# Optimization experiments

Hardware: AMD Instinct MI355X
Metric: run time of the kernel (lower is better)

The kernel has to match this reference:

```python
import jax, jax.numpy as jnp
import numpy as np

# Dimensions: batch B, window W (time features), nodes M, hidden HID, hops NLAYERS
B, W, M, HID, NLAYERS = 32, 168, 2048, 128, 6


def setup_inputs() -> dict:
    key = jax.random.key(0)
    ks = jax.random.split(key, 6)
    x = jax.random.normal(ks[0], (B, W, M), dtype=jnp.float32)
    # scale L so matrix powers L^k stay bounded (spectral radius < 1)
    L = jax.random.normal(ks[1], (M, M), dtype=jnp.float32) / (2.0 * np.float32(np.sqrt(M)))
    # stacked per-hop MLP params: linears[i]: W->HID, linears2[i]: HID->1
    W1 = jax.random.normal(ks[2], (NLAYERS + 1, HID, W), dtype=jnp.float32) / np.float32(np.sqrt(W))
    b1 = jax.random.normal(ks[3], (NLAYERS + 1, HID), dtype=jnp.float32) * 0.01
    W2 = jax.random.normal(ks[4], (NLAYERS + 1, HID), dtype=jnp.float32) / np.float32(np.sqrt(HID))
    b2 = jax.random.normal(ks[5], (NLAYERS + 1,), dtype=jnp.float32) * 0.01
    return {"x": x, "L": L, "W1": W1, "b1": b1, "W2": W2, "b2": b2}


def _hop_mlp(t, w1, bb1, w2, bb2):
    # t: [B, M, W] -> scalar score per node: Linear(W->HID), ReLU, Linear(HID->1)
    h = jax.nn.relu(jnp.einsum('bmw,hw->bmh', t, w1) + bb1)
    return jnp.einsum('bmh,h->bm', h, w2) + bb2


def reference(x, L, W1, b1, W2, b2):
    xt = jnp.swapaxes(x, 1, 2)  # [B, M, W] (x.transpose(2,1))
    s = _hop_mlp(xt, W1[0], b1[0], W2[0], b2[0])  # [B, M]
    P = L
    for i in range(1, NLAYERS + 1):
        # PP.expand + bmm == broadcasted matmul; never materialize [B,M,M]
        t = jnp.einsum('ij,bjw->biw', P, xt)  # [B, M, W]
        s = s + _hop_mlp(t, W1[i], b1[i], W2[i], b2[i])
        P = jnp.matmul(L, P)  # next graph power
    return s  # [B, M]; output_fun is None so no final nonlinearity
```

## Files before the change

kernel.cpp:

```cpp
#include <hip/hip_runtime.h>
#include <cstdint>
#include <cstddef>

typedef __bf16 bf16_t;
typedef __attribute__((ext_vector_type(8))) __bf16 bf16x8;
typedef __attribute__((ext_vector_type(4))) __bf16 bf16x4;
typedef __attribute__((ext_vector_type(4))) float floatx4;

#define NB 32
#define NW 168
#define NM 2048
#define NHID 128
#define NBW (NB * NW)

#define GLOAD_LDS16(g, l)                                          \
  __builtin_amdgcn_global_load_lds(                                \
      (const __attribute__((address_space(1))) void*)(g),          \
      (__attribute__((address_space(3))) void*)(l), 16, 0, 0)

__global__ void cast_bf16_kernel(const float* __restrict__ in, bf16_t* __restrict__ out, int n4) {
  int stride = gridDim.x * blockDim.x;
  for (int i = blockIdx.x * blockDim.x + threadIdx.x; i < n4; i += stride) {
    float4 v = ((const float4*)in)[i];
    bf16x4 o = {(bf16_t)v.x, (bf16_t)v.y, (bf16_t)v.z, (bf16_t)v.w};
    ((bf16x4*)out)[i] = o;
  }
}

__global__ void prep_x_kernel(const float* __restrict__ x, bf16_t* __restrict__ Xb,
                              bf16_t* __restrict__ XT) {
  __shared__ float tile[64][65];
  const int R = NBW, C = NM;
  int r0 = blockIdx.y * 64, c0 = blockIdx.x * 64;
  int t = threadIdx.x;
  int tr = t >> 4, tc4 = (t & 15) * 4;
#pragma unroll
  for (int p = 0; p < 4; ++p) {
    int row = p * 16 + tr;
    float4 v = *(const float4*)(x + (size_t)(r0 + row) * C + c0 + tc4);
    tile[row][tc4 + 0] = v.x;
    tile[row][tc4 + 1] = v.y;
    tile[row][tc4 + 2] = v.z;
    tile[row][tc4 + 3] = v.w;
    bf16x4 o = {(bf16_t)v.x, (bf16_t)v.y, (bf16_t)v.z, (bf16_t)v.w};
    *(bf16x4*)(Xb + (size_t)(r0 + row) * C + c0 + tc4) = o;
  }
  __syncthreads();
#pragma unroll
  for (int p = 0; p < 4; ++p) {
    int c = p * 16 + tr;
    bf16x4 o = {(bf16_t)tile[tc4 + 0][c], (bf16_t)tile[tc4 + 1][c],
                (bf16_t)tile[tc4 + 2][c], (bf16_t)tile[tc4 + 3][c]};
    *(bf16x4*)(XT + (size_t)(c0 + c) * R + r0 + tc4) = o;
  }
}

__global__ void gemm_nt_kernel(const bf16_t* __restrict__ A, const bf16_t* __restrict__ Bt,
                               bf16_t* __restrict__ C, bf16_t* __restrict__ Ct,
                               int K, int lda, int ldb, int ldc, int ldct, int write_c) {
  __shared__ bf16_t As[128 * 32];
  __shared__ bf16_t Bs[128 * 32];
  int tid = threadIdx.x;
  int m0 = blockIdx.y * 128, n0 = blockIdx.x * 128;
  int lane = tid & 63, wv = tid >> 6;
  int wm = wv >> 1, wn = wv & 1;
  int quad = lane >> 4, l15 = lane & 15;

  int p0 = wv * 128 + lane;
  int p1 = p0 + 64;
  int row0 = p0 >> 2, kc0 = (p0 & 3) ^ ((p0 >> 3) & 3);
  int row1 = p1 >> 2, kc1 = (p1 & 3) ^ ((p1 >> 3) & 3);
  const bf16_t* a0p = A + (size_t)(m0 + row0) * lda + kc0 * 8;
  const bf16_t* a1p = A + (size_t)(m0 + row1) * lda + kc1 * 8;
  const bf16_t* b0p = Bt + (size_t)(n0 + row0) * ldb + kc0 * 8;
  const bf16_t* b1p = Bt + (size_t)(n0 + row1) * ldb + kc1 * 8;
  bf16_t* As_d0 = As + (size_t)(wv * 128) * 8;
  bf16_t* As_d1 = As + (size_t)(wv * 128 + 64) * 8;
  bf16_t* Bs_d0 = Bs + (size_t)(wv * 128) * 8;
  bf16_t* Bs_d1 = Bs + (size_t)(wv * 128 + 64) * 8;

  int swz = (l15 >> 1) & 3;
  int kpos = (quad ^ swz) * 8;

  floatx4 zero4 = {0.f, 0.f, 0.f, 0.f};
  floatx4 acc[4][4];
#pragma unroll
  for (int mi = 0; mi < 4; ++mi)
#pragma unroll
    for (int ni = 0; ni < 4; ++ni) acc[mi][ni] = zero4;

  for (int kb = 0; kb < K; kb += 32) {
    GLOAD_LDS16(a0p + kb, As_d0);
    GLOAD_LDS16(a1p + kb, As_d1);
    GLOAD_LDS16(b0p + kb, Bs_d0);
    GLOAD_LDS16(b1p + kb, Bs_d1);
    __syncthreads();
    bf16x8 af[4], bf[4];
#pragma unroll
    for (int mi = 0; mi < 4; ++mi)
      af[mi] = *(const bf16x8*)(As + (wm * 64 + mi * 16 + l15) * 32 + kpos);
#pragma unroll
    for (int ni = 0; ni < 4; ++ni)
      bf[ni] = *(const bf16x8*)(Bs + (wn * 64 + ni * 16 + l15) * 32 + kpos);
#pragma unroll
    for (int mi = 0; mi < 4; ++mi)
#pragma unroll
      for (int ni = 0; ni < 4; ++ni)
        acc[mi][ni] = __builtin_amdgcn_mfma_f32_16x16x32_bf16(af[mi], bf[ni], acc[mi][ni], 0, 0, 0);
    __syncthreads();
  }
#pragma unroll
  for (int mi = 0; mi < 4; ++mi) {
#pragma unroll
    for (int ni = 0; ni < 4; ++ni) {
      int col = n0 + wn * 64 + ni * 16 + l15;
      int rowb = m0 + wm * 64 + mi * 16 + quad * 4;
      bf16x4 tv;
#pragma unroll
      for (int r = 0; r < 4; ++r) tv[r] = (bf16_t)acc[mi][ni][r];
      *(bf16x4*)(Ct + (size_t)col * ldct + rowb) = tv;
      if (write_c) {
#pragma unroll
        for (int r = 0; r < 4; ++r)
          C[(size_t)(rowb + r) * ldc + col] = tv[r];
      }
    }
  }
}

__global__ void mlp_score_kernel(const bf16_t* __restrict__ T, const bf16_t* __restrict__ W1b,
                                 const float* __restrict__ b1, const float* __restrict__ W2,
                                 const float* __restrict__ b2, float* __restrict__ out,
                                 int hop, int accumulate) {
  __shared__ bf16_t Bs[24 * 128 * 8];
  __shared__ float sred[4][64];
  const bf16_t* Wh = W1b + (size_t)hop * NHID * NW;
  const float* b1h = b1 + hop * NHID;
  const float* w2h = W2 + hop * NHID;
  int tid = threadIdx.x;
  int r0 = blockIdx.x * 128;
  int lane = tid & 63, wv = tid >> 6;
  int wm = wv >> 1, wn = wv & 1;
  int quad = lane >> 4, l15 = lane & 15;

  for (int c = 2688 + tid; c < 3072; c += 256) {
    int4 z = {0, 0, 0, 0};
    *(int4*)(Bs + (size_t)c * 8) = z;
  }
  for (int i = 0; i < 11; ++i) {
    int c = i * 256 + tid;
    if (c < 2688) {
      int kc = c >> 7;
      int h = (c & 127) ^ ((kc & 3) << 2);
      GLOAD_LDS16(Wh + (size_t)h * NW + kc * 8, Bs + (size_t)(i * 256 + wv * 64) * 8);
    }
  }

  const bf16_t* arow[4];
#pragma unroll
  for (int mi = 0; mi < 4; ++mi) {
    int R = r0 + wm * 64 + mi * 16 + l15;
    arow[mi] = T + (size_t)(R >> 5) * NBW + (size_t)(R & 31) * NW + quad * 8;
  }

  floatx4 zero4 = {0.f, 0.f, 0.f, 0.f};
  floatx4 acc[4][4];
#pragma unroll
  for (int mi = 0; mi < 4; ++mi)
#pragma unroll
    for (int ni = 0; ni < 4; ++ni) acc[mi][ni] = zero4;

  __syncthreads();

#pragma unroll
  for (int kb = 0; kb < 192; kb += 32) {
    int kc = (kb >> 3) + quad;
    bf16x8 af[4], bf[4];
#pragma unroll
    for (int mi = 0; mi < 4; ++mi)
      af[mi] = *(const bf16x8*)(arow[mi] + kb);
#pragma unroll
    for (int ni = 0; ni < 4; ++ni) {
      int hpos = (wn * 64 + ni * 16 + l15) ^ ((kc & 3) << 2);
      bf[ni] = *(const bf16x8*)(Bs + (size_t)(kc * 128 + hpos) * 8);
    }
#pragma unroll
    for (int mi = 0; mi < 4; ++mi)
#pragma unroll
      for (int ni = 0; ni < 4; ++ni)
        acc[mi][ni] = __builtin_amdgcn_mfma_f32_16x16x32_bf16(af[mi], bf[ni], acc[mi][ni], 0, 0, 0);
  }

  float part[4][4];
#pragma unroll
  for (int mi = 0; mi < 4; ++mi)
#pragma unroll
    for (int r = 0; r < 4; ++r) part[mi][r] = 0.f;
#pragma unroll
  for (int ni = 0; ni < 4; ++ni) {
    int col = wn * 64 + ni * 16 + l15;
    float b1v = b1h[col];
    float w2v = w2h[col];
#pragma unroll
    for (int mi = 0; mi < 4; ++mi)
#pragma unroll
      for (int r = 0; r < 4; ++r) {
        float h = acc[mi][ni][r] + b1v;
        h = h > 0.f ? h : 0.f;
        part[mi][r] += h * w2v;
      }
  }
#pragma unroll
  for (int off = 1; off < 16; off <<= 1)
#pragma unroll
    for (int mi = 0; mi < 4; ++mi)
#pragma unroll
      for (int r = 0; r < 4; ++r) part[mi][r] += __shfl_xor(part[mi][r], off);
  if (l15 == 0) {
#pragma unroll
    for (int mi = 0; mi < 4; ++mi)
#pragma unroll
      for (int r = 0; r < 4; ++r) sred[wv][mi * 16 + quad * 4 + r] = part[mi][r];
  }
  __syncthreads();
  if (tid < 128) {
    int half = tid >> 6;
    int lr = tid & 63;
    float v = sred[half * 2][lr] + sred[half * 2 + 1][lr] + b2[hop];
    int R = r0 + half * 64 + lr;
    int idx = (R & 31) * NM + (R >> 5);
    if (accumulate)
      out[idx] += v;
    else
      out[idx] = v;
  }
}

extern "C" void kernel_launch(void* const* d_in, const int* in_sizes, int n_in,
                              void* d_out, int out_size, void* d_ws, size_t ws_size,
                              hipStream_t stream) {
  const float* x = (const float*)d_in[0];
  const float* L = (const float*)d_in[1];
  const float* W1 = (const float*)d_in[2];
  const float* b1 = (const float*)d_in[3];
  const float* W2 = (const float*)d_in[4];
  const float* b2 = (const float*)d_in[5];
  float* out = (float*)d_out;

  char* ws = (char*)d_ws;
  size_t off = 0;
  auto walloc = [&](size_t bytes) -> void* {
    off = (off + 255) & ~(size_t)255;
    void* p = ws + off;
    off += bytes;
    return p;
  };
  bf16_t* Xb = (bf16_t*)walloc((size_t)NBW * NM * 2);
  bf16_t* XT = (bf16_t*)walloc((size_t)NM * NBW * 2);
  bf16_t* Lb = (bf16_t*)walloc((size_t)NM * NM * 2);
  bf16_t* W1b = (bf16_t*)walloc((size_t)7 * NHID * NW * 2);
  bf16_t* Ta = (bf16_t*)walloc((size_t)NBW * NM * 2);
  (void)ws_size; (void)in_sizes; (void)n_in; (void)out_size;

  prep_x_kernel<<<dim3(NM / 64, NBW / 64), dim3(256), 0, stream>>>(x, Xb, XT);
  cast_bf16_kernel<<<dim3(1024), dim3(256), 0, stream>>>(L, Lb, NM * NM / 4);
  cast_bf16_kernel<<<dim3(64), dim3(256), 0, stream>>>(W1, W1b, 7 * NHID * NW / 4);

  mlp_score_kernel<<<dim3(NM * NB / 128), dim3(256), 0, stream>>>(XT, W1b, b1, W2, b2, out, 0, 0);

  bf16_t* src = Xb;
  bf16_t* dst = Ta;
  for (int i = 1; i <= 6; ++i) {
    gemm_nt_kernel<<<dim3(NM / 128, NBW / 128), dim3(256), 0, stream>>>(
        src, Lb, dst, XT, NM, NM, NM, NM, NBW, (i < 6) ? 1 : 0);
    mlp_score_kernel<<<dim3(NM * NB / 128), dim3(256), 0, stream>>>(XT, W1b, b1, W2, b2, out, i, 1);
    bf16_t* t = src; src = dst; dst = t;
  }
}
```

Before: 552.7 us.

## Batch hops by precomputing powers of L and fusing multi-hop GEMMs and MLPs

Replaces the six sequential propagation GEMMs with three wider launches. It computes L^2 and L^3 on spare blocks and multiplies by a stacked [L, L^2, L^3] so several hops come out of one GEMM. The MLP scoring is batched over two or three hops per launch and accumulates with atomicAdd into a zero-initialised output. This cuts serial dependency depth and launch count and gives the GPU larger grids, at the cost of extra GEMM work for the matrix powers. It also adds extra bf16 rounding through the precomputed powers.

```diff
diff --git a/kernel.cpp b/kernel.cpp
--- a/kernel.cpp
+++ b/kernel.cpp
@@ -24,6 +24,31 @@
     float4 v = ((const float4*)in)[i];
     bf16x4 o = {(bf16_t)v.x, (bf16_t)v.y, (bf16_t)v.z, (bf16_t)v.w};
     ((bf16x4*)out)[i] = o;
+  }
+}
+
+__global__ void transpose_cast_kernel(const float* __restrict__ in, bf16_t* __restrict__ out,
+                                      int R, int C) {
+  __shared__ float tile[64][65];
+  int r0 = blockIdx.y * 64, c0 = blockIdx.x * 64;
+  int t = threadIdx.x;
+  int tr = t >> 4, tc4 = (t & 15) * 4;
+#pragma unroll
+  for (int p = 0; p < 4; ++p) {
+    int row = p * 16 + tr;
+    float4 v = *(const float4*)(in + (size_t)(r0 + row) * C + c0 + tc4);
+    tile[row][tc4 + 0] = v.x;
+    tile[row][tc4 + 1] = v.y;
+    tile[row][tc4 + 2] = v.z;
+    tile[row][tc4 + 3] = v.w;
+  }
+  __syncthreads();
+#pragma unroll
+  for (int p = 0; p < 4; ++p) {
+    int c = p * 16 + tr;
+    bf16x4 o = {(bf16_t)tile[tc4 + 0][c], (bf16_t)tile[tc4 + 1][c],
+                (bf16_t)tile[tc4 + 2][c], (bf16_t)tile[tc4 + 3][c]};
+    *(bf16x4*)(out + (size_t)(c0 + c) * R + r0 + tc4) = o;
   }
 }
 
@@ -55,13 +80,35 @@
   }
 }
 
-__global__ void gemm_nt_kernel(const bf16_t* __restrict__ A, const bf16_t* __restrict__ Bt,
-                               bf16_t* __restrict__ C, bf16_t* __restrict__ Ct,
-                               int K, int lda, int ldb, int ldc, int ldct, int write_c) {
+template <int MODE>
+__global__ void gemm_multi(const bf16_t* __restrict__ A, const bf16_t* __restrict__ Bt,
+                           const bf16_t* __restrict__ A2, const bf16_t* __restrict__ Bt2,
+                           bf16_t* __restrict__ C, bf16_t* __restrict__ Caux,
+                           bf16_t* __restrict__ Ct0, bf16_t* __restrict__ Ct1,
+                           bf16_t* __restrict__ Ct2) {
+  constexpr int NBX = (MODE == 0) ? 16 : (MODE == 1) ? 32 : 48;
+  constexpr int NMAIN = 42 * NBX;
   __shared__ bf16_t As[128 * 32];
   __shared__ bf16_t Bs[128 * 32];
+  int bid = blockIdx.x;
   int tid = threadIdx.x;
-  int m0 = blockIdx.y * 128, n0 = blockIdx.x * 128;
+  const bf16_t* Ap;
+  const bf16_t* Btp;
+  int m0, n0;
+  bool aux = false;
+  if (MODE < 2 && bid >= NMAIN) {
+    aux = true;
+    int l = bid - NMAIN;
+    m0 = (l >> 4) * 128;
+    n0 = (l & 15) * 128;
+    Ap = A2;
+    Btp = Bt2;
+  } else {
+    m0 = (bid / NBX) * 128;
+    n0 = (bid % NBX) * 128;
+    Ap = A;
+    Btp = Bt;
+  }
   int lane = tid & 63, wv = tid >> 6;
   int wm = wv >> 1, wn = wv & 1;
   int quad = lane >> 4, l15 = lane & 15;
@@ -70,10 +117,10 @@
   int p1 = p0 + 64;
   int row0 = p0 >> 2, kc0 = (p0 & 3) ^ ((p0 >> 3) & 3);
   int row1 = p1 >> 2, kc1 = (p1 & 3) ^ ((p1 >> 3) & 3);
-  const bf16_t* a0p = A + (size_t)(m0 + row0) * lda + kc0 * 8;
-  const bf16_t* a1p = A + (size_t)(m0 + row1) * lda + kc1 * 8;
-  const bf16_t* b0p = Bt + (size_t)(n0 + row0) * ldb + kc0 * 8;
-  const bf16_t* b1p = Bt + (size_t)(n0 + row1) * ldb + kc1 * 8;
+  const bf16_t* a0p = Ap + (size_t)(m0 + row0) * 2048 + kc0 * 8;
+  const bf16_t* a1p = Ap + (size_t)(m0 + row1) * 2048 + kc1 * 8;
+  const bf16_t* b0p = Btp + (size_t)(n0 + row0) * 2048 + kc0 * 8;
+  const bf16_t* b1p = Btp + (size_t)(n0 + row1) * 2048 + kc1 * 8;
   bf16_t* As_d0 = As + (size_t)(wv * 128) * 8;
   bf16_t* As_d1 = As + (size_t)(wv * 128 + 64) * 8;
   bf16_t* Bs_d0 = Bs + (size_t)(wv * 128) * 8;
@@ -89,7 +136,7 @@
 #pragma unroll
     for (int ni = 0; ni < 4; ++ni) acc[mi][ni] = zero4;
 
-  for (int kb = 0; kb < K; kb += 32) {
+  for (int kb = 0; kb < 2048; kb += 32) {
     GLOAD_LDS16(a0p + kb, As_d0);
     GLOAD_LDS16(a1p + kb, As_d1);
     GLOAD_LDS16(b0p + kb, Bs_d0);
@@ -109,36 +156,50 @@
         acc[mi][ni] = __builtin_amdgcn_mfma_f32_16x16x32_bf16(af[mi], bf[ni], acc[mi][ni], 0, 0, 0);
     __syncthreads();
   }
+
+  int nh = n0 >> 11;
+  int n0l = n0 - (nh << 11);
+  bf16_t* Ctp = nullptr;
+  bf16_t* Cp = nullptr;
+  if (aux) {
+    Cp = Caux;
+  } else {
+    Ctp = (nh == 0) ? Ct0 : (nh == 1) ? Ct1 : Ct2;
+    if (MODE == 0) Cp = C;
+    if (MODE == 1 && nh == 1) Cp = C;
+  }
 #pragma unroll
   for (int mi = 0; mi < 4; ++mi) {
 #pragma unroll
     for (int ni = 0; ni < 4; ++ni) {
-      int col = n0 + wn * 64 + ni * 16 + l15;
+      int col_l = n0l + wn * 64 + ni * 16 + l15;
       int rowb = m0 + wm * 64 + mi * 16 + quad * 4;
       bf16x4 tv;
 #pragma unroll
       for (int r = 0; r < 4; ++r) tv[r] = (bf16_t)acc[mi][ni][r];
-      *(bf16x4*)(Ct + (size_t)col * ldct + rowb) = tv;
-      if (write_c) {
-#pragma unroll
-        for (int r = 0; r < 4; ++r)
-          C[(size_t)(rowb + r) * ldc + col] = tv[r];
+      if (Ctp) *(bf16x4*)(Ctp + (size_t)col_l * NBW + rowb) = tv;
+      if (Cp) {
+#pragma unroll
+        for (int r = 0; r < 4; ++r) Cp[(size_t)(rowb + r) * 2048 + col_l] = tv[r];
       }
     }
   }
 }
 
-__global__ void mlp_score_kernel(const bf16_t* __restrict__ T, const bf16_t* __restrict__ W1b,
-                                 const float* __restrict__ b1, const float* __restrict__ W2,
-                                 const float* __restrict__ b2, float* __restrict__ out,
-                                 int hop, int accumulate) {
+__global__ void mlp_multi(const bf16_t* __restrict__ T0, const bf16_t* __restrict__ T1,
+                          const bf16_t* __restrict__ T2, const bf16_t* __restrict__ W1b,
+                          const float* __restrict__ b1, const float* __restrict__ W2,
+                          const float* __restrict__ b2, float* __restrict__ out, int hop_base) {
   __shared__ bf16_t Bs[24 * 128 * 8];
   __shared__ float sred[4][64];
+  int sub = blockIdx.x >> 9;
+  int r0 = (blockIdx.x & 511) * 128;
+  int hop = hop_base + sub;
+  const bf16_t* T = (sub == 0) ? T0 : (sub == 1) ? T1 : T2;
   const bf16_t* Wh = W1b + (size_t)hop * NHID * NW;
   const float* b1h = b1 + hop * NHID;
   const float* w2h = W2 + hop * NHID;
   int tid = threadIdx.x;
-  int r0 = blockIdx.x * 128;
   int lane = tid & 63, wv = tid >> 6;
   int wm = wv >> 1, wn = wv & 1;
   int quad = lane >> 4, l15 = lane & 15;
@@ -229,10 +290,7 @@
     float v = sred[half * 2][lr] + sred[half * 2 + 1][lr] + b2[hop];
     int R = r0 + half * 64 + lr;
     int idx = (R & 31) * NM + (R >> 5);
-    if (accumulate)
-      out[idx] += v;
-    else
-      out[idx] = v;
+    atomicAdd(out + idx, v);
   }
 }
 
@@ -255,25 +313,35 @@
     off += bytes;
     return p;
   };
-  bf16_t* Xb = (bf16_t*)walloc((size_t)NBW * NM * 2);
-  bf16_t* XT = (bf16_t*)walloc((size_t)NM * NBW * 2);
-  bf16_t* Lb = (bf16_t*)walloc((size_t)NM * NM * 2);
+  const size_t SZ_L = (size_t)NM * NM * 2;
+  const size_t SZ_T = (size_t)NBW * NM * 2;
   bf16_t* W1b = (bf16_t*)walloc((size_t)7 * NHID * NW * 2);
-  bf16_t* Ta = (bf16_t*)walloc((size_t)NBW * NM * 2);
-  (void)ws_size; (void)in_sizes; (void)n_in; (void)out_size;
-
-  prep_x_kernel<<<dim3(NM / 64, NBW / 64), dim3(256), 0, stream>>>(x, Xb, XT);
+  bf16_t* Lstack = (bf16_t*)walloc(3 * SZ_L);
+  bf16_t* Lb = Lstack;
+  bf16_t* L2b = Lstack + (size_t)NM * NM;
+  bf16_t* L3b = Lstack + 2 * (size_t)NM * NM;
+  bf16_t* Ltb = (bf16_t*)walloc(SZ_L);
+  bf16_t* Tt1 = (bf16_t*)walloc(SZ_T);
+  bf16_t* XTp2 = (bf16_t*)((char*)Ltb);
+  bf16_t* Xb = (bf16_t*)walloc(SZ_T);
+  bf16_t* Tt3 = Xb;
+  bf16_t* XTp0 = (bf16_t*)walloc(SZ_T);
+  bf16_t* XTp1 = (bf16_t*)walloc(SZ_T);
+  (void)ws_size; (void)in_sizes; (void)n_in;
+
+  hipMemsetAsync(out, 0, (size_t)out_size * 4, stream);
+  prep_x_kernel<<<dim3(NM / 64, NBW / 64), dim3(256), 0, stream>>>(x, Xb, XTp0);
   cast_bf16_kernel<<<dim3(1024), dim3(256), 0, stream>>>(L, Lb, NM * NM / 4);
+  transpose_cast_kernel<<<dim3(NM / 64, NM / 64), dim3(256), 0, stream>>>(L, Ltb, NM, NM);
   cast_bf16_kernel<<<dim3(64), dim3(256), 0, stream>>>(W1, W1b, 7 * NHID * NW / 4);
 
-  mlp_score_kernel<<<dim3(NM * NB / 128), dim3(256), 0, stream>>>(XT, W1b, b1, W2, b2, out, 0, 0);
-
-  bf16_t* src = Xb;
-  bf16_t* dst = Ta;
-  for (int i = 1; i <= 6; ++i) {
-    gemm_nt_kernel<<<dim3(NM / 128, NBW / 128), dim3(256), 0, stream>>>(
-        src, Lb, dst, XT, NM, NM, NM, NM, NBW, (i < 6) ? 1 : 0);
-    mlp_score_kernel<<<dim3(NM * NB / 128), dim3(256), 0, stream>>>(XT, W1b, b1, W2, b2, out, i, 1);
-    bf16_t* t = src; src = dst; dst = t;
-  }
-}
+  gemm_multi<0><<<dim3(928), dim3(256), 0, stream>>>(
+      Xb, Lb, Lb, Ltb, Tt1, L2b, XTp1, nullptr, nullptr);
+  mlp_multi<<<dim3(1024), dim3(256), 0, stream>>>(XTp0, XTp1, nullptr, W1b, b1, W2, b2, out, 0);
+  gemm_multi<1><<<dim3(1600), dim3(256), 0, stream>>>(
+      Tt1, Lstack, L2b, Ltb, Tt3, L3b, XTp0, XTp1, nullptr);
+  mlp_multi<<<dim3(1024), dim3(256), 0, stream>>>(XTp0, XTp1, nullptr, W1b, b1, W2, b2, out, 2);
+  gemm_multi<2><<<dim3(2016), dim3(256), 0, stream>>>(
+      Tt3, Lstack, nullptr, nullptr, nullptr, nullptr, XTp0, XTp1, XTp2);
+  mlp_multi<<<dim3(1536), dim3(256), 0, stream>>>(XTp0, XTp1, XTp2, W1b, b1, W2, b2, out, 4);
+}
```

Measured after the change: 561.6 us. No clear change (+1.6%).

## Overlap each hop's GEMM with previous hop's MLP scoring in one launch

Applied to the files above, without the earlier changes.

Merges the three prep kernels into one launch and repacks W1 into a zero-padded 192-wide bf16 layout. Each hop now runs one kernel where the first 672 blocks compute the next graph-propagation GEMM while the remaining 512 blocks score the previous hop's output through the MLP. XT buffers are double-buffered so both halves can run at once. This cuts the launch count and fills idle CUs during the GEMM, at the cost of extra workspace and MLP blocks that read W1 straight from global memory instead of staging it in LDS.

```diff
diff --git a/kernel.cpp b/kernel.cpp
--- a/kernel.cpp
+++ b/kernel.cpp
@@ -12,76 +12,85 @@
 #define NM 2048
 #define NHID 128
 #define NBW (NB * NW)
+#define GEMM_BLOCKS 672
 
 #define GLOAD_LDS16(g, l)                                          \
   __builtin_amdgcn_global_load_lds(                                \
       (const __attribute__((address_space(1))) void*)(g),          \
       (__attribute__((address_space(3))) void*)(l), 16, 0, 0)
 
-__global__ void cast_bf16_kernel(const float* __restrict__ in, bf16_t* __restrict__ out, int n4) {
-  int stride = gridDim.x * blockDim.x;
-  for (int i = blockIdx.x * blockDim.x + threadIdx.x; i < n4; i += stride) {
-    float4 v = ((const float4*)in)[i];
-    bf16x4 o = {(bf16_t)v.x, (bf16_t)v.y, (bf16_t)v.z, (bf16_t)v.w};
-    ((bf16x4*)out)[i] = o;
+__global__ void prep_all(const float* __restrict__ x, bf16_t* __restrict__ Xb,
+                         bf16_t* __restrict__ XT, const float* __restrict__ L,
+                         bf16_t* __restrict__ Lb, const float* __restrict__ W1,
+                         bf16_t* __restrict__ W1p) {
+  __shared__ float tile[64][65];
+  int bid = blockIdx.x;
+  int t = threadIdx.x;
+  if (bid < 2688) {
+    const int C = NM;
+    int r0 = (bid >> 5) * 64, c0 = (bid & 31) * 64;
+    int tr = t >> 4, tc4 = (t & 15) * 4;
+#pragma unroll
+    for (int p = 0; p < 4; ++p) {
+      int row = p * 16 + tr;
+      float4 v = *(const float4*)(x + (size_t)(r0 + row) * C + c0 + tc4);
+      tile[row][tc4 + 0] = v.x;
+      tile[row][tc4 + 1] = v.y;
+      tile[row][tc4 + 2] = v.z;
+      tile[row][tc4 + 3] = v.w;
+      bf16x4 o = {(bf16_t)v.x, (bf16_t)v.y, (bf16_t)v.z, (bf16_t)v.w};
+      *(bf16x4*)(Xb + (size_t)(r0 + row) * C + c0 + tc4) = o;
+    }
+    __syncthreads();
+#pragma unroll
+    for (int p = 0; p < 4; ++p) {
+      int c = p * 16 + tr;
+      bf16x4 o = {(bf16_t)tile[tc4 + 0][c], (bf16_t)tile[tc4 + 1][c],
+                  (bf16_t)tile[tc4 + 2][c], (bf16_t)tile[tc4 + 3][c]};
+      *(bf16x4*)(XT + (size_t)(c0 + c) * NBW + r0 + tc4) = o;
+    }
+  } else if (bid < 3200) {
+    int i = (bid - 2688) * 256 + t;
+    const int n4 = NM * NM / 4;
+    const int stride = 512 * 256;
+    for (; i < n4; i += stride) {
+      float4 v = ((const float4*)L)[i];
+      bf16x4 o = {(bf16_t)v.x, (bf16_t)v.y, (bf16_t)v.z, (bf16_t)v.w};
+      ((bf16x4*)Lb)[i] = o;
+    }
+  } else {
+    int hop = bid - 3200;
+    const float* src = W1 + (size_t)hop * NHID * NW;
+    bf16_t* dst = W1p + (size_t)hop * NHID * 192;
+    for (int c = t; c < 3072; c += 256) {
+      int h = c / 24, kc = c % 24;
+      bf16x8 o;
+      if (kc < 21) {
+        const float* s = src + (size_t)h * NW + kc * 8;
+#pragma unroll
+        for (int j = 0; j < 8; ++j) o[j] = (bf16_t)s[j];
+      } else {
+#pragma unroll
+        for (int j = 0; j < 8; ++j) o[j] = (bf16_t)0.0f;
+      }
+      *(bf16x8*)(dst + (size_t)h * 192 + kc * 8) = o;
+    }
   }
 }
 
-__global__ void prep_x_kernel(const float* __restrict__ x, bf16_t* __restrict__ Xb,
-                              bf16_t* __restrict__ XT) {
-  __shared__ float tile[64][65];
-  const int R = NBW, C = NM;
-  int r0 = blockIdx.y * 64, c0 = blockIdx.x * 64;
-  int t = threadIdx.x;
-  int tr = t >> 4, tc4 = (t & 15) * 4;
-#pragma unroll
-  for (int p = 0; p < 4; ++p) {
-    int row = p * 16 + tr;
-    float4 v = *(const float4*)(x + (size_t)(r0 + row) * C + c0 + tc4);
-    tile[row][tc4 + 0] = v.x;
-    tile[row][tc4 + 1] = v.y;
-    tile[row][tc4 + 2] = v.z;
-    tile[row][tc4 + 3] = v.w;
-    bf16x4 o = {(bf16_t)v.x, (bf16_t)v.y, (bf16_t)v.z, (bf16_t)v.w};
-    *(bf16x4*)(Xb + (size_t)(r0 + row) * C + c0 + tc4) = o;
-  }
-  __syncthreads();
-#pragma unroll
-  for (int p = 0; p < 4; ++p) {
-    int c = p * 16 + tr;
-    bf16x4 o = {(bf16_t)tile[tc4 + 0][c], (bf16_t)tile[tc4 + 1][c],
-                (bf16_t)tile[tc4 + 2][c], (bf16_t)tile[tc4 + 3][c]};
-    *(bf16x4*)(XT + (size_t)(c0 + c) * R + r0 + tc4) = o;
-  }
-}
-
-__global__ void gemm_nt_kernel(const bf16_t* __restrict__ A, const bf16_t* __restrict__ Bt,
-                               bf16_t* __restrict__ C, bf16_t* __restrict__ Ct,
-                               int K, int lda, int ldb, int ldc, int ldct, int write_c) {
+__global__ void fused_hop(const bf16_t* __restrict__ A, const bf16_t* __restrict__ Lb,
+                          bf16_t* __restrict__ Tt, bf16_t* __restrict__ XTout,
+                          const bf16_t* __restrict__ XTin, const bf16_t* __restrict__ W1p,
+                          const float* __restrict__ b1, const float* __restrict__ W2,
+                          const float* __restrict__ b2, float* __restrict__ out,
+                          int hop, int accumulate, int gemm_blocks, int write_c) {
   __shared__ bf16_t As[128 * 32];
   __shared__ bf16_t Bs[128 * 32];
+  __shared__ float sred[4][64];
   int tid = threadIdx.x;
-  int m0 = blockIdx.y * 128, n0 = blockIdx.x * 128;
   int lane = tid & 63, wv = tid >> 6;
   int wm = wv >> 1, wn = wv & 1;
   int quad = lane >> 4, l15 = lane & 15;
-
-  int p0 = wv * 128 + lane;
-  int p1 = p0 + 64;
-  int row0 = p0 >> 2, kc0 = (p0 & 3) ^ ((p0 >> 3) & 3);
-  int row1 = p1 >> 2, kc1 = (p1 & 3) ^ ((p1 >> 3) & 3);
-  const bf16_t* a0p = A + (size_t)(m0 + row0) * lda + kc0 * 8;
-  const bf16_t* a1p = A + (size_t)(m0 + row1) * lda + kc1 * 8;
-  const bf16_t* b0p = Bt + (size_t)(n0 + row0) * ldb + kc0 * 8;
-  const bf16_t* b1p = Bt + (size_t)(n0 + row1) * ldb + kc1 * 8;
-  bf16_t* As_d0 = As + (size_t)(wv * 128) * 8;
-  bf16_t* As_d1 = As + (size_t)(wv * 128 + 64) * 8;
-  bf16_t* Bs_d0 = Bs + (size_t)(wv * 128) * 8;
-  bf16_t* Bs_d1 = Bs + (size_t)(wv * 128 + 64) * 8;
-
-  int swz = (l15 >> 1) & 3;
-  int kpos = (quad ^ swz) * 8;
-
   floatx4 zero4 = {0.f, 0.f, 0.f, 0.f};
   floatx4 acc[4][4];
 #pragma unroll
@@ -89,150 +98,135 @@
 #pragma unroll
     for (int ni = 0; ni < 4; ++ni) acc[mi][ni] = zero4;
 
-  for (int kb = 0; kb < K; kb += 32) {
-    GLOAD_LDS16(a0p + kb, As_d0);
-    GLOAD_LDS16(a1p + kb, As_d1);
-    GLOAD_LDS16(b0p + kb, Bs_d0);
-    GLOAD_LDS16(b1p + kb, Bs_d1);
+  if ((int)blockIdx.x < gemm_blocks) {
+    int bid = blockIdx.x;
+    int m0 = (bid >> 4) * 128, n0 = (bid & 15) * 128;
+    int p0 = wv * 128 + lane;
+    int p1 = p0 + 64;
+    int row0 = p0 >> 2, kc0 = (p0 & 3) ^ ((p0 >> 3) & 3);
+    int row1 = p1 >> 2, kc1 = (p1 & 3) ^ ((p1 >> 3) & 3);
+    const bf16_t* a0p = A + (size_t)(m0 + row0) * NM + kc0 * 8;
+    const bf16_t* a1p = A + (size_t)(m0 + row1) * NM + kc1 * 8;
+    const bf16_t* b0p = Lb + (size_t)(n0 + row0) * NM + kc0 * 8;
+    const bf16_t* b1p = Lb + (size_t)(n0 + row1) * NM + kc1 * 8;
+    bf16_t* As_d0 = As + (size_t)(wv * 128) * 8;
+    bf16_t* As_d1 = As + (size_t)(wv * 128 + 64) * 8;
+    bf16_t* Bs_d0 = Bs + (size_t)(wv * 128) * 8;
+    bf16_t* Bs_d1 = Bs + (size_t)(wv * 128 + 64) * 8;
+    int swz = (l15 >> 1) & 3;
+    int kpos = (quad ^ swz) * 8;
+
+    for (int kb = 0; kb < 2048; kb += 32) {
+      GLOAD_LDS16(a0p + kb, As_d0);
+      GLOAD_LDS16(a1p + kb, As_d1);
+      GLOAD_LDS16(b0p + kb, Bs_d0);
+      GLOAD_LDS16(b1p + kb, Bs_d1);
+      __syncthreads();
+      bf16x8 af[4], bf[4];
+#pragma unroll
+      for (int mi = 0; mi < 4; ++mi)
+        af[mi] = *(const bf16x8*)(As + (wm * 64 + mi * 16 + l15) * 32 + kpos);
+#pragma unroll
+      for (int ni = 0; ni < 4; ++ni)
+        bf[ni] = *(const bf16x8*)(Bs + (wn * 64 + ni * 16 + l15) * 32 + kpos);
+#pragma unroll
+      for (int mi = 0; mi < 4; ++mi)
+#pragma unroll
+        for (int ni = 0; ni < 4; ++ni)
+          acc[mi][ni] =
+              __builtin_amdgcn_mfma_f32_16x16x32_bf16(af[mi], bf[ni], acc[mi][ni], 0, 0, 0);
+      __syncthreads();
+    }
+#pragma unroll
+    for (int mi = 0; mi < 4; ++mi) {
+#pragma unroll
+      for (int ni = 0; ni < 4; ++ni) {
+        int col = n0 + wn * 64 + ni * 16 + l15;
+        int rowb = m0 + wm * 64 + mi * 16 + quad * 4;
+        bf16x4 tv;
+#pragma unroll
+        for (int r = 0; r < 4; ++r) tv[r] = (bf16_t)acc[mi][ni][r];
+        *(bf16x4*)(XTout + (size_t)col * NBW + rowb) = tv;
+        if (write_c) {
+#pragma unroll
+          for (int r = 0; r < 4; ++r) Tt[(size_t)(rowb + r) * NM + col] = tv[r];
+        }
+      }
+    }
+  } else {
+    int bid2 = blockIdx.x - gemm_blocks;
+    int r0 = bid2 * 128;
+    const bf16_t* Wh = W1p + (size_t)hop * NHID * 192;
+    const float* b1h = b1 + hop * NHID;
+    const float* w2h = W2 + hop * NHID;
+    const bf16_t* arow[4];
+#pragma unroll
+    for (int mi = 0; mi < 4; ++mi) {
+      int R = r0 + wm * 64 + mi * 16 + l15;
+      arow[mi] = XTin + (size_t)(R >> 5) * NBW + (size_t)(R & 31) * NW + quad * 8;
+    }
+#pragma unroll
+    for (int kb = 0; kb < 192; kb += 32) {
+      int kc = (kb >> 3) + quad;
+      bf16x8 af[4], bf[4];
+#pragma unroll
+      for (int mi = 0; mi < 4; ++mi)
+        af[mi] = *(const bf16x8*)(arow[mi] + kb);
+#pragma unroll
+      for (int ni = 0; ni < 4; ++ni) {
+        int h = wn * 64 + ni * 16 + l15;
+        bf[ni] = *(const bf16x8*)(Wh + (size_t)h * 192 + kc * 8);
+      }
+#pragma unroll
+      for (int mi = 0; mi < 4; ++mi)
+#pragma unroll
+        for (int ni = 0; ni < 4; ++ni)
+          acc[mi][ni] =
+              __builtin_amdgcn_mfma_f32_16x16x32_bf16(af[mi], bf[ni], acc[mi][ni], 0, 0, 0);
+    }
+    float part[4][4];
+#pragma unroll
+    for (int mi = 0; mi < 4; ++mi)
+#pragma unroll
+      for (int r = 0; r < 4; ++r) part[mi][r] = 0.f;
+#pragma unroll
+    for (int ni = 0; ni < 4; ++ni) {
+      int col = wn * 64 + ni * 16 + l15;
+      float b1v = b1h[col];
+      float w2v = w2h[col];
+#pragma unroll
+      for (int mi = 0; mi < 4; ++mi)
+#pragma unroll
+        for (int r = 0; r < 4; ++r) {
+          float h = acc[mi][ni][r] + b1v;
+          h = h > 0.f ? h : 0.f;
+          part[mi][r] += h * w2v;
+        }
+    }
+#pragma unroll
+    for (int off = 1; off < 16; off <<= 1)
+#pragma unroll
+      for (int mi = 0; mi < 4; ++mi)
+#pragma unroll
+        for (int r = 0; r < 4; ++r) part[mi][r] += __shfl_xor(part[mi][r], off);
+    if (l15 == 0) {
+#pragma unroll
+      for (int mi = 0; mi < 4; ++mi)
+#pragma unroll
+        for (int r = 0; r < 4; ++r) sred[wv][mi * 16 + quad * 4 + r] = part[mi][r];
+    }
     __syncthreads();
-    bf16x8 af[4], bf[4];
-#pragma unroll
-    for (int mi = 0; mi < 4; ++mi)
-      af[mi] = *(const bf16x8*)(As + (wm * 64 + mi * 16 + l15) * 32 + kpos);
-#pragma unroll
-    for (int ni = 0; ni < 4; ++ni)
-      bf[ni] = *(const bf16x8*)(Bs + (wn * 64 + ni * 16 + l15) * 32 + kpos);
-#pragma unroll
-    for (int mi = 0; mi < 4; ++mi)
-#pragma unroll
-      for (int ni = 0; ni < 4; ++ni)
-        acc[mi][ni] = __builtin_amdgcn_mfma_f32_16x16x32_bf16(af[mi], bf[ni], acc[mi][ni], 0, 0, 0);
-    __syncthreads();
-  }
-#pragma unroll
-  for (int mi = 0; mi < 4; ++mi) {
-#pragma unroll
-    for (int ni = 0; ni < 4; ++ni) {
-      int col = n0 + wn * 64 + ni * 16 + l15;
-      int rowb = m0 + wm * 64 + mi * 16 + quad * 4;
-      bf16x4 tv;
-#pragma unroll
-      for (int r = 0; r < 4; ++r) tv[r] = (bf16_t)acc[mi][ni][r];
-      *(bf16x4*)(Ct + (size_t)col * ldct + rowb) = tv;
-      if (write_c) {
-#pragma unroll
-        for (int r = 0; r < 4; ++r)
-          C[(size_t)(rowb + r) * ldc + col] = tv[r];
-      }
-    }
-  }
-}
-
-__global__ void mlp_score_kernel(const bf16_t* __restrict__ T, const bf16_t* __restrict__ W1b,
-                                 const float* __restrict__ b1, const float* __restrict__ W2,
-                                 const float* __restrict__ b2, float* __restrict__ out,
-                                 int hop, int accumulate) {
-  __shared__ bf16_t Bs[24 * 128 * 8];
-  __shared__ float sred[4][64];
-  const bf16_t* Wh = W1b + (size_t)hop * NHID * NW;
-  const float* b1h = b1 + hop * NHID;
-  const float* w2h = W2 + hop * NHID;
-  int tid = threadIdx.x;
-  int r0 = blockIdx.x * 128;
-  int lane = tid & 63, wv = tid >> 6;
-  int wm = wv >> 1, wn = wv & 1;
-  int quad = lane >> 4, l15 = lane & 15;
-
-  for (int c = 2688 + tid; c < 3072; c += 256) {
-    int4 z = {0, 0, 0, 0};
-    *(int4*)(Bs + (size_t)c * 8) = z;
-  }
-  for (int i = 0; i < 11; ++i) {
-    int c = i * 256 + tid;
-    if (c < 2688) {
-      int kc = c >> 7;
-      int h = (c & 127) ^ ((kc & 3) << 2);
-      GLOAD_LDS16(Wh + (size_t)h * NW + kc * 8, Bs + (size_t)(i * 256 + wv * 64) * 8);
-    }
-  }
-
-  const bf16_t* arow[4];
-#pragma unroll
-  for (int mi = 0; mi < 4; ++mi) {
-    int R = r0 + wm * 64 + mi * 16 + l15;
-    arow[mi] = T + (size_t)(R >> 5) * NBW + (size_t)(R & 31) * NW + quad * 8;
-  }
-
-  floatx4 zero4 = {0.f, 0.f, 0.f, 0.f};
-  floatx4 acc[4][4];
-#pragma unroll
-  for (int mi = 0; mi < 4; ++mi)
-#pragma unroll
-    for (int ni = 0; ni < 4; ++ni) acc[mi][ni] = zero4;
-
-  __syncthreads();
-
-#pragma unroll
-  for (int kb = 0; kb < 192; kb += 32) {
-    int kc = (kb >> 3) + quad;
-    bf16x8 af[4], bf[4];
-#pragma unroll
-    for (int mi = 0; mi < 4; ++mi)
-      af[mi] = *(const bf16x8*)(arow[mi] + kb);
-#pragma unroll
-    for (int ni = 0; ni < 4; ++ni) {
-      int hpos = (wn * 64 + ni * 16 + l15) ^ ((kc & 3) << 2);
-      bf[ni] = *(const bf16x8*)(Bs + (size_t)(kc * 128 + hpos) * 8);
-    }
-#pragma unroll
-    for (int mi = 0; mi < 4; ++mi)
-#pragma unroll
-      for (int ni = 0; ni < 4; ++ni)
-        acc[mi][ni] = __builtin_amdgcn_mfma_f32_16x16x32_bf16(af[mi], bf[ni], acc[mi][ni], 0, 0, 0);
-  }
-
-  float part[4][4];
-#pragma unroll
-  for (int mi = 0; mi < 4; ++mi)
-#pragma unroll
-    for (int r = 0; r < 4; ++r) part[mi][r] = 0.f;
-#pragma unroll
-  for (int ni = 0; ni < 4; ++ni) {
-    int col = wn * 64 + ni * 16 + l15;
-    float b1v = b1h[col];
-    float w2v = w2h[col];
-#pragma unroll
-    for (int mi = 0; mi < 4; ++mi)
-#pragma unroll
-      for (int r = 0; r < 4; ++r) {
-        float h = acc[mi][ni][r] + b1v;
-        h = h > 0.f ? h : 0.f;
-        part[mi][r] += h * w2v;
-      }
-  }
-#pragma unroll
-  for (int off = 1; off < 16; off <<= 1)
-#pragma unroll
-    for (int mi = 0; mi < 4; ++mi)
-#pragma unroll
-      for (int r = 0; r < 4; ++r) part[mi][r] += __shfl_xor(part[mi][r], off);
-  if (l15 == 0) {
-#pragma unroll
-    for (int mi = 0; mi < 4; ++mi)
-#pragma unroll
-      for (int r = 0; r < 4; ++r) sred[wv][mi * 16 + quad * 4 + r] = part[mi][r];
-  }
-  __syncthreads();
-  if (tid < 128) {
-    int half = tid >> 6;
-    int lr = tid & 63;
-    float v = sred[half * 2][lr] + sred[half * 2 + 1][lr] + b2[hop];
-    int R = r0 + half * 64 + lr;
-    int idx = (R & 31) * NM + (R >> 5);
-    if (accumulate)
-      out[idx] += v;
-    else
-      out[idx] = v;
+    if (tid < 128) {
+      int half = tid >> 6;
+      int lr = tid & 63;
+      float v = sred[half * 2][lr] + sred[half * 2 + 1][lr] + b2[hop];
+      int R = r0 + half * 64 + lr;
+      int idx = (R & 31) * NM + (R >> 5);
+      if (accumulate)
+        out[idx] += v;
+      else
+        out[idx] = v;
+    }
   }
 }
 
@@ -255,25 +249,31 @@
     off += bytes;
     return p;
   };
-  bf16_t* Xb = (bf16_t*)walloc((size_t)NBW * NM * 2);
-  bf16_t* XT = (bf16_t*)walloc((size_t)NM * NBW * 2);
+  const size_t SZ_T = (size_t)NBW * NM * 2;
+  bf16_t* W1p = (bf16_t*)walloc((size_t)7 * NHID * 192 * 2);
   bf16_t* Lb = (bf16_t*)walloc((size_t)NM * NM * 2);
-  bf16_t* W1b = (bf16_t*)walloc((size_t)7 * NHID * NW * 2);
-  bf16_t* Ta = (bf16_t*)walloc((size_t)NBW * NM * 2);
+  bf16_t* Xb = (bf16_t*)walloc(SZ_T);
+  bf16_t* Tta = (bf16_t*)walloc(SZ_T);
+  bf16_t* Ttb = (bf16_t*)walloc(SZ_T);
+  bf16_t* XTa = (bf16_t*)walloc(SZ_T);
+  bf16_t* XTb = (bf16_t*)walloc(SZ_T);
+  walloc(4096);
   (void)ws_size; (void)in_sizes; (void)n_in; (void)out_size;
 
-  prep_x_kernel<<<dim3(NM / 64, NBW / 64), dim3(256), 0, stream>>>(x, Xb, XT);
-  cast_bf16_kernel<<<dim3(1024), dim3(256), 0, stream>>>(L, Lb, NM * NM / 4);
-  cast_bf16_kernel<<<dim3(64), dim3(256), 0, stream>>>(W1, W1b, 7 * NHID * NW / 4);
-
-  mlp_score_kernel<<<dim3(NM * NB / 128), dim3(256), 0, stream>>>(XT, W1b, b1, W2, b2, out, 0, 0);
-
-  bf16_t* src = Xb;
-  bf16_t* dst = Ta;
-  for (int i = 1; i <= 6; ++i) {
-    gemm_nt_kernel<<<dim3(NM / 128, NBW / 128), dim3(256), 0, stream>>>(
-        src, Lb, dst, XT, NM, NM, NM, NM, NBW, (i < 6) ? 1 : 0);
-    mlp_score_kernel<<<dim3(NM * NB / 128), dim3(256), 0, stream>>>(XT, W1b, b1, W2, b2, out, i, 1);
-    bf16_t* t = src; src = dst; dst = t;
-  }
+  prep_all<<<dim3(3207), dim3(256), 0, stream>>>(x, Xb, XTa, L, Lb, W1, W1p);
+
+  fused_hop<<<dim3(GEMM_BLOCKS + 512), dim3(256), 0, stream>>>(
+      Xb, Lb, Tta, XTb, XTa, W1p, b1, W2, b2, out, 0, 0, GEMM_BLOCKS, 1);
+  fused_hop<<<dim3(GEMM_BLOCKS + 512), dim3(256), 0, stream>>>(
+      Tta, Lb, Ttb, XTa, XTb, W1p, b1, W2, b2, out, 1, 1, GEMM_BLOCKS, 1);
+  fused_hop<<<dim3(GEMM_BLOCKS + 512), dim3(256), 0, stream>>>(
+      Ttb, Lb, Tta, XTb, XTa, W1p, b1, W2, b2, out, 2, 1, GEMM_BLOCKS, 1);
+  fused_hop<<<dim3(GEMM_BLOCKS + 512), dim3(256), 0, stream>>>(
+      Tta, Lb, Ttb, XTa, XTb, W1p, b1, W2, b2, out, 3, 1, GEMM_BLOCKS, 1);
+  fused_hop<<<dim3(GEMM_BLOCKS + 512), dim3(256), 0, stream>>>(
+      Ttb, Lb, Tta, XTb, XTa, W1p, b1, W2, b2, out, 4, 1, GEMM_BLOCKS, 1);
+  fused_hop<<<dim3(GEMM_BLOCKS + 512), dim3(256), 0, stream>>>(
+      Tta, Lb, Ttb, XTa, XTb, W1p, b1, W2, b2, out, 5, 1, GEMM_BLOCKS, 0);
+  fused_hop<<<dim3(512), dim3(256), 0, stream>>>(
+      Ttb, Lb, Tta, XTb, XTa, W1p, b1, W2, b2, out, 6, 1, 0, 0);
 }
```

New measurement: 563.2 us. About the same (+1.9%).
